# Performance work log

Measured on AMD Instinct MI355X. Metric: run time of the kernel, lower is better.

The kernel has to match this reference:

```python
import jax, jax.numpy as jnp
import numpy as np

S, N, D = 8, 2048, 256

def setup_inputs() -> dict:
    key = jax.random.key(0)
    k0, k1, k2 = jax.random.split(key, 3)
    tensor0 = jax.random.normal(k0, (S, N, D), dtype=jnp.float32)
    tensor1 = jax.random.normal(k1, (S, N, D), dtype=jnp.float32)
    # glorot-ish scale for the (D, D) bilinear kernel
    kernel = jax.random.normal(k2, (D, D), dtype=jnp.float32) * (1.0 / np.sqrt(D))
    bias = jnp.zeros((1,), dtype=jnp.float32)  # scalar bias, shape () in keras
    return {"tensor0": tensor0, "tensor1": tensor1, "kernel": kernel, "bias": bias}

def reference(tensor0, tensor1, kernel, bias):
    # Faithful math of Bilinear(bilin_axes=[1]) on inputs [S, N, D]:
    # out[s, i, j] = sum_{d,e} tensor1[s,i,d] * kernel[d,e] * tensor0[s,j,e] + bias
    # (the original builds the full [S,N,S,N] cross tensor and extracts the
    #  batch diagonal; this einsum is the equivalent O(S*N*N*D) contraction).
    qt0 = jnp.einsum('de,sje->sjd', kernel, tensor0)      # [S, N, D]
    out = jnp.einsum('sid,sjd->sij', tensor1, qt0)        # [S, N, N]
    return out + bias[0]
```

## Files before the change

### kernel.cpp

```cpp
#include <hip/hip_runtime.h>
#include <hip/hip_bf16.h>


typedef __bf16 bf16x8 __attribute__((ext_vector_type(8)));
typedef float f32x4 __attribute__((ext_vector_type(4)));

__device__ __forceinline__ unsigned short f2bf(float f) {
  union { __hip_bfloat16 h; unsigned short u; } v;
  v.h = __float2bfloat16(f);
  return v.u;
}

__global__ __launch_bounds__(256) void cvt3(const float4* __restrict__ t0,
                                            const float4* __restrict__ t1,
                                            const float4* __restrict__ kk,
                                            ushort4* __restrict__ o0,
                                            ushort4* __restrict__ o1,
                                            ushort4* __restrict__ ok) {
  const int stride = gridDim.x * blockDim.x;
  const int i0 = blockIdx.x * blockDim.x + threadIdx.x;
  for (int j = i0; j < 1048576; j += stride) {
    float4 v = t0[j];
    o0[j] = make_ushort4(f2bf(v.x), f2bf(v.y), f2bf(v.z), f2bf(v.w));
  }
  for (int j = i0; j < 1048576; j += stride) {
    float4 v = t1[j];
    o1[j] = make_ushort4(f2bf(v.x), f2bf(v.y), f2bf(v.z), f2bf(v.w));
  }
  for (int j = i0; j < 16384; j += stride) {
    float4 v = kk[j];
    ok[j] = make_ushort4(f2bf(v.x), f2bf(v.y), f2bf(v.z), f2bf(v.w));
  }
}

template <bool OUT_BF16>
__global__ __launch_bounds__(256, 2) void gemm_nt(
    const unsigned short* __restrict__ A, const unsigned short* __restrict__ B,
    void* __restrict__ Cout, const float* __restrict__ bias,
    const int K, const int ldc,
    const long long aStride, const long long bStride, const long long cStride) {
  __shared__ unsigned short sA[2][128 * 64];
  __shared__ unsigned short sB[2][128 * 64];

  const int tid = threadIdx.x;
  const int wave = tid >> 6;
  const int lane = tid & 63;
  const int quad = lane >> 4;
  const int l16 = lane & 15;
  const int wrow = (wave >> 1) * 64;
  const int wcol = (wave & 1) * 64;
  const int rsw = (l16 & 7) * 8;

  const int brow = blockIdx.y * 128;
  const int bcol = blockIdx.x * 128;
  const long long bz = blockIdx.z;

  const unsigned short* Ab = A + bz * aStride + (long long)brow * K;
  const unsigned short* Bb = B + bz * bStride + (long long)bcol * K;

  const int srow = lane >> 3;
  const int scol = ((lane & 7) ^ srow) * 8;

  auto stage = [&](unsigned short* dA, unsigned short* dB, int kt) {
#pragma unroll
    for (int i = 0; i < 4; i++) {
      const int r = i * 32 + wave * 8;
      const unsigned short* ga = Ab + (long long)(r + srow) * K + kt + scol;
      const unsigned short* gb = Bb + (long long)(r + srow) * K + kt + scol;
      __builtin_amdgcn_global_load_lds(
          (const __attribute__((address_space(1))) unsigned int*)ga,
          (__attribute__((address_space(3))) unsigned int*)(dA + r * 64),
          16, 0, 0);
      __builtin_amdgcn_global_load_lds(
          (const __attribute__((address_space(1))) unsigned int*)gb,
          (__attribute__((address_space(3))) unsigned int*)(dB + r * 64),
          16, 0, 0);
    }
  };

  f32x4 acc[4][4];
#pragma unroll
  for (int i = 0; i < 4; i++)
#pragma unroll
    for (int j = 0; j < 4; j++) acc[i][j] = (f32x4){0.f, 0.f, 0.f, 0.f};

  stage(sA[0], sB[0], 0);

  int cur = 0;
  for (int kt = 0; kt < K; kt += 64) {
    __syncthreads();
    const unsigned short* a = sA[cur];
    const unsigned short* b = sB[cur];
    {
      bf16x8 af[4], bfr[4];
#pragma unroll
      for (int mi = 0; mi < 4; mi++) {
        const int row = wrow + mi * 16 + l16;
        af[mi] = *(const bf16x8*)&a[row * 64 + ((quad * 8) ^ rsw)];
      }
#pragma unroll
      for (int ni = 0; ni < 4; ni++) {
        const int row = wcol + ni * 16 + l16;
        bfr[ni] = *(const bf16x8*)&b[row * 64 + ((quad * 8) ^ rsw)];
      }
      if (kt + 64 < K) stage(sA[cur ^ 1], sB[cur ^ 1], kt + 64);
#pragma unroll
      for (int mi = 0; mi < 4; mi++)
#pragma unroll
        for (int ni = 0; ni < 4; ni++)
          acc[mi][ni] = __builtin_amdgcn_mfma_f32_16x16x32_bf16(
              af[mi], bfr[ni], acc[mi][ni], 0, 0, 0);
    }
    {
      bf16x8 af[4], bfr[4];
#pragma unroll
      for (int mi = 0; mi < 4; mi++) {
        const int row = wrow + mi * 16 + l16;
        af[mi] = *(const bf16x8*)&a[row * 64 + ((32 + quad * 8) ^ rsw)];
      }
#pragma unroll
      for (int ni = 0; ni < 4; ni++) {
        const int row = wcol + ni * 16 + l16;
        bfr[ni] = *(const bf16x8*)&b[row * 64 + ((32 + quad * 8) ^ rsw)];
      }
#pragma unroll
      for (int mi = 0; mi < 4; mi++)
#pragma unroll
        for (int ni = 0; ni < 4; ni++)
          acc[mi][ni] = __builtin_amdgcn_mfma_f32_16x16x32_bf16(
              af[mi], bfr[ni], acc[mi][ni], 0, 0, 0);
    }
    cur ^= 1;
  }

  if constexpr (OUT_BF16) {
    unsigned short* C = (unsigned short*)Cout + bz * cStride;
#pragma unroll
    for (int mi = 0; mi < 4; mi++)
#pragma unroll
      for (int ni = 0; ni < 4; ni++) {
        const int r0 = brow + wrow + mi * 16 + quad * 4;
        const int c = bcol + wcol + ni * 16 + l16;
#pragma unroll
        for (int r = 0; r < 4; r++)
          C[(long long)(r0 + r) * ldc + c] = f2bf(acc[mi][ni][r]);
      }
  } else {
    const float bv = bias[0];
    float* C = (float*)Cout + bz * cStride;
#pragma unroll
    for (int mi = 0; mi < 4; mi++)
#pragma unroll
      for (int ni = 0; ni < 4; ni++) {
        const int r0 = brow + wrow + mi * 16 + quad * 4;
        const int c = bcol + wcol + ni * 16 + l16;
#pragma unroll
        for (int r = 0; r < 4; r++)
          C[(long long)(r0 + r) * ldc + c] = acc[mi][ni][r] + bv;
      }
  }
}

extern "C" void kernel_launch(void* const* d_in, const int* in_sizes, int n_in,
                              void* d_out, int out_size, void* d_ws, size_t ws_size,
                              hipStream_t stream) {
  const float* t0 = (const float*)d_in[0];
  const float* t1 = (const float*)d_in[1];
  const float* kk = (const float*)d_in[2];
  const float* bias = (const float*)d_in[3];

  unsigned short* T0b = (unsigned short*)d_ws;
  unsigned short* T1b = T0b + 4194304;
  unsigned short* Kb = T1b + 4194304;
  unsigned short* Qb = Kb + 65536;

  cvt3<<<4096, 256, 0, stream>>>((const float4*)t0, (const float4*)t1,
                                 (const float4*)kk, (ushort4*)T0b,
                                 (ushort4*)T1b, (ushort4*)Kb);

  gemm_nt<true><<<dim3(2, 128, 1), 256, 0, stream>>>(T0b, Kb, Qb, nullptr, 256,
                                                     256, 0, 0, 0);

  gemm_nt<false><<<dim3(16, 16, 8), 256, 0, stream>>>(
      T1b, Qb, d_out, bias, 256, 2048, 524288LL, 524288LL, 4194304LL);
}
```

Baseline: 184.9 us.

## Fuse fp32-to-bf16 conversion into first GEMM and merge with tensor1 conversion

Replaces the separate conversion kernel and first GEMM with one prep kernel. Blocks 0-255 compute Q = tensor0·kernelᵀ, loading fp32 tiles directly and converting them to bf16 while writing to LDS. The remaining 1024 blocks convert tensor1 to bf16. This removes one launch and the bf16 round trip for tensor0 and the kernel. The cost is that the fused GEMM's staging now goes through registers with synchronous loads rather than async global_load_lds, and the GEMM and conversion blocks compete for the same CUs.

```diff
diff --git a/kernel.cpp b/kernel.cpp
--- a/kernel.cpp
+++ b/kernel.cpp
@@ -11,26 +11,115 @@
   return v.u;
 }
 
-__global__ __launch_bounds__(256) void cvt3(const float4* __restrict__ t0,
-                                            const float4* __restrict__ t1,
-                                            const float4* __restrict__ kk,
-                                            ushort4* __restrict__ o0,
-                                            ushort4* __restrict__ o1,
-                                            ushort4* __restrict__ ok) {
-  const int stride = gridDim.x * blockDim.x;
-  const int i0 = blockIdx.x * blockDim.x + threadIdx.x;
-  for (int j = i0; j < 1048576; j += stride) {
-    float4 v = t0[j];
-    o0[j] = make_ushort4(f2bf(v.x), f2bf(v.y), f2bf(v.z), f2bf(v.w));
-  }
-  for (int j = i0; j < 1048576; j += stride) {
-    float4 v = t1[j];
-    o1[j] = make_ushort4(f2bf(v.x), f2bf(v.y), f2bf(v.z), f2bf(v.w));
-  }
-  for (int j = i0; j < 16384; j += stride) {
-    float4 v = kk[j];
-    ok[j] = make_ushort4(f2bf(v.x), f2bf(v.y), f2bf(v.z), f2bf(v.w));
-  }
+__device__ __forceinline__ void cvt8_store(unsigned short* dst, const float* src) {
+  float4 v0 = *(const float4*)src;
+  float4 v1 = *(const float4*)(src + 4);
+  union { unsigned short u[8]; uint4 q; } p;
+  p.u[0] = f2bf(v0.x); p.u[1] = f2bf(v0.y); p.u[2] = f2bf(v0.z); p.u[3] = f2bf(v0.w);
+  p.u[4] = f2bf(v1.x); p.u[5] = f2bf(v1.y); p.u[6] = f2bf(v1.z); p.u[7] = f2bf(v1.w);
+  *(uint4*)dst = p.q;
+}
+
+__global__ __launch_bounds__(256, 2) void prep(
+    const float* __restrict__ t0, const float4* __restrict__ t1,
+    const float* __restrict__ kk, ushort4* __restrict__ T1b,
+    unsigned short* __restrict__ Qb) {
+  const int tid = threadIdx.x;
+
+  if (blockIdx.x >= 256) {
+    const int i0 = (blockIdx.x - 256) * 256 + tid;
+#pragma unroll
+    for (int it = 0; it < 4; it++) {
+      const int j = i0 + it * 262144;
+      float4 v = t1[j];
+      T1b[j] = make_ushort4(f2bf(v.x), f2bf(v.y), f2bf(v.z), f2bf(v.w));
+    }
+    return;
+  }
+
+  __shared__ unsigned short sA[2][128 * 64];
+  __shared__ unsigned short sB[2][128 * 64];
+
+  const int wave = tid >> 6;
+  const int lane = tid & 63;
+  const int quad = lane >> 4;
+  const int l16 = lane & 15;
+  const int wrow = (wave >> 1) * 64;
+  const int wcol = (wave & 1) * 64;
+  const int rsw = (l16 & 7) * 8;
+
+  const int brow = (blockIdx.x >> 1) * 128;
+  const int bcol = (blockIdx.x & 1) * 128;
+
+  const float* Af = t0 + (long long)brow * 256;
+  const float* Bf = kk + (long long)bcol * 256;
+
+  const int srow = lane >> 3;
+  const int scol = ((lane & 7) ^ srow) * 8;
+
+  auto stage1 = [&](unsigned short* dA, unsigned short* dB, int kt) {
+#pragma unroll
+    for (int i = 0; i < 4; i++) {
+      const int rr = i * 32 + wave * 8 + srow;
+      cvt8_store(dA + rr * 64 + (lane & 7) * 8,
+                 Af + (long long)rr * 256 + kt + scol);
+      cvt8_store(dB + rr * 64 + (lane & 7) * 8,
+                 Bf + (long long)rr * 256 + kt + scol);
+    }
+  };
+
+  f32x4 acc[4][4];
+#pragma unroll
+  for (int i = 0; i < 4; i++)
+#pragma unroll
+    for (int j = 0; j < 4; j++) acc[i][j] = (f32x4){0.f, 0.f, 0.f, 0.f};
+
+  stage1(sA[0], sB[0], 0);
+
+  int cur = 0;
+  for (int kt = 0; kt < 256; kt += 64) {
+    __syncthreads();
+    const unsigned short* a = sA[cur];
+    const unsigned short* b = sB[cur];
+    bf16x8 af[4], bfr[4];
+#pragma unroll
+    for (int mi = 0; mi < 4; mi++)
+      af[mi] = *(const bf16x8*)&a[(wrow + mi * 16 + l16) * 64 + ((quad * 8) ^ rsw)];
+#pragma unroll
+    for (int ni = 0; ni < 4; ni++)
+      bfr[ni] = *(const bf16x8*)&b[(wcol + ni * 16 + l16) * 64 + ((quad * 8) ^ rsw)];
+    if (kt + 64 < 256) stage1(sA[cur ^ 1], sB[cur ^ 1], kt + 64);
+#pragma unroll
+    for (int mi = 0; mi < 4; mi++)
+#pragma unroll
+      for (int ni = 0; ni < 4; ni++)
+        acc[mi][ni] = __builtin_amdgcn_mfma_f32_16x16x32_bf16(
+            af[mi], bfr[ni], acc[mi][ni], 0, 0, 0);
+#pragma unroll
+    for (int mi = 0; mi < 4; mi++)
+      af[mi] = *(const bf16x8*)&a[(wrow + mi * 16 + l16) * 64 + ((32 + quad * 8) ^ rsw)];
+#pragma unroll
+    for (int ni = 0; ni < 4; ni++)
+      bfr[ni] = *(const bf16x8*)&b[(wcol + ni * 16 + l16) * 64 + ((32 + quad * 8) ^ rsw)];
+#pragma unroll
+    for (int mi = 0; mi < 4; mi++)
+#pragma unroll
+      for (int ni = 0; ni < 4; ni++)
+        acc[mi][ni] = __builtin_amdgcn_mfma_f32_16x16x32_bf16(
+            af[mi], bfr[ni], acc[mi][ni], 0, 0, 0);
+    cur ^= 1;
+  }
+
+#pragma unroll
+  for (int mi = 0; mi < 4; mi++)
+#pragma unroll
+    for (int ni = 0; ni < 4; ni++) {
+      const int r0 = brow + wrow + mi * 16 + quad * 4;
+      const int c = bcol + wcol + ni * 16 + l16;
+#pragma unroll
+      for (int r = 0; r < 4; r++)
+        Qb[(long long)(r0 + r) * 256 + c] = f2bf(acc[mi][ni][r]);
+    }
 }
 
 template <bool OUT_BF16>
@@ -94,15 +183,11 @@
     {
       bf16x8 af[4], bfr[4];
 #pragma unroll
-      for (int mi = 0; mi < 4; mi++) {
-        const int row = wrow + mi * 16 + l16;
-        af[mi] = *(const bf16x8*)&a[row * 64 + ((quad * 8) ^ rsw)];
-      }
-#pragma unroll
-      for (int ni = 0; ni < 4; ni++) {
-        const int row = wcol + ni * 16 + l16;
-        bfr[ni] = *(const bf16x8*)&b[row * 64 + ((quad * 8) ^ rsw)];
-      }
+      for (int mi = 0; mi < 4; mi++)
+        af[mi] = *(const bf16x8*)&a[(wrow + mi * 16 + l16) * 64 + ((quad * 8) ^ rsw)];
+#pragma unroll
+      for (int ni = 0; ni < 4; ni++)
+        bfr[ni] = *(const bf16x8*)&b[(wcol + ni * 16 + l16) * 64 + ((quad * 8) ^ rsw)];
       if (kt + 64 < K) stage(sA[cur ^ 1], sB[cur ^ 1], kt + 64);
 #pragma unroll
       for (int mi = 0; mi < 4; mi++)
@@ -114,15 +199,11 @@
     {
       bf16x8 af[4], bfr[4];
 #pragma unroll
-      for (int mi = 0; mi < 4; mi++) {
-        const int row = wrow + mi * 16 + l16;
-        af[mi] = *(const bf16x8*)&a[row * 64 + ((32 + quad * 8) ^ rsw)];
-      }
-#pragma unroll
-      for (int ni = 0; ni < 4; ni++) {
-        const int row = wcol + ni * 16 + l16;
-        bfr[ni] = *(const bf16x8*)&b[row * 64 + ((32 + quad * 8) ^ rsw)];
-      }
+      for (int mi = 0; mi < 4; mi++)
+        af[mi] = *(const bf16x8*)&a[(wrow + mi * 16 + l16) * 64 + ((32 + quad * 8) ^ rsw)];
+#pragma unroll
+      for (int ni = 0; ni < 4; ni++)
+        bfr[ni] = *(const bf16x8*)&b[(wcol + ni * 16 + l16) * 64 + ((32 + quad * 8) ^ rsw)];
 #pragma unroll
       for (int mi = 0; mi < 4; mi++)
 #pragma unroll
@@ -169,17 +250,10 @@
   const float* kk = (const float*)d_in[2];
   const float* bias = (const float*)d_in[3];
 
-  unsigned short* T0b = (unsigned short*)d_ws;
-  unsigned short* T1b = T0b + 4194304;
-  unsigned short* Kb = T1b + 4194304;
-  unsigned short* Qb = Kb + 65536;
-
-  cvt3<<<4096, 256, 0, stream>>>((const float4*)t0, (const float4*)t1,
-                                 (const float4*)kk, (ushort4*)T0b,
-                                 (ushort4*)T1b, (ushort4*)Kb);
-
-  gemm_nt<true><<<dim3(2, 128, 1), 256, 0, stream>>>(T0b, Kb, Qb, nullptr, 256,
-                                                     256, 0, 0, 0);
+  unsigned short* T1b = (unsigned short*)d_ws;
+  unsigned short* Qb = T1b + 4194304;
+
+  prep<<<1280, 256, 0, stream>>>(t0, (const float4*)t1, kk, (ushort4*)T1b, Qb);
 
   gemm_nt<false><<<dim3(16, 16, 8), 256, 0, stream>>>(
       T1b, Qb, d_out, bias, 256, 2048, 524288LL, 524288LL, 4194304LL);
```

After: 180.3 us. 2.5% less time.
